# Kernel tuning notes

Hardware: AMD Instinct MI355X
Metric: run time of the kernel (lower is better)

## Reference

```python
import jax, jax.numpy as jnp
import numpy as np

N_NODES = 50000
N_EDGES = 800000
D_IN = 128
HEADS = 8
UNITS = 16


def setup_inputs() -> dict:
    key = jax.random.key(0)
    ks = jax.random.split(key, 6)
    x = jax.random.normal(ks[0], (N_NODES, D_IN), dtype=jnp.float32)
    edges = jax.random.randint(ks[1], (N_EDGES, 2), 0, N_NODES, dtype=jnp.int32)
    # glorot_uniform-style init for kernels
    lim_k = float(np.sqrt(6.0 / (D_IN + HEADS * UNITS)))
    kernel = jax.random.uniform(ks[2], (D_IN, HEADS, UNITS), minval=-lim_k, maxval=lim_k, dtype=jnp.float32)
    lim_a = float(np.sqrt(6.0 / (1 + HEADS * UNITS)))
    kernel_attention1 = jax.random.uniform(ks[3], (1, HEADS, UNITS), minval=-lim_a, maxval=lim_a, dtype=jnp.float32)
    bias_attention = jnp.zeros((1, HEADS, UNITS), dtype=jnp.float32)
    bias = jnp.zeros((HEADS * UNITS,), dtype=jnp.float32)
    return {"x": x, "edges": edges, "kernel": kernel,
            "kernel_attention1": kernel_attention1,
            "bias_attention": bias_attention, "bias": bias}


def reference(x, edges, kernel, kernel_attention1, bias_attention, bias):
    # GATv2 (version=2), merge_type='concat', use_bias=True, training=False
    n_nodes = x.shape[0]
    sources = edges[:, 0]
    targets = edges[:, 1]

    xp = jnp.einsum('nd,dhu->nhu', x, kernel)          # [N, H, U]
    xbias = xp + bias_attention                        # [N, H, U]

    # per-edge attention score: leaky_relu(x_t + x_s) . a   (GATv2)
    s = jax.nn.leaky_relu(xbias[targets] + xbias[sources], negative_slope=0.2)  # [E, H, U]
    scores = jnp.sum(s * kernel_attention1, axis=-1)   # [E, H]

    # segment softmax over incoming edges of each target node
    smax = jax.ops.segment_max(scores, targets, num_segments=n_nodes)  # [N, H]
    scores = jnp.exp(scores - smax[targets])
    ssum = jax.ops.segment_sum(scores, targets, num_segments=n_nodes)  # [N, H]
    scores = scores / (ssum[targets] + 1e-7)           # [E, H]

    # weighted scatter-aggregate of source features
    out = jax.ops.segment_sum(scores[..., None] * xp[sources], targets,
                              num_segments=n_nodes)    # [N, H, U]
    out = out.reshape(n_nodes, HEADS * UNITS) + bias   # concat heads
    return jax.nn.gelu(out, approximate=True)
```

## Files before the change

### kernel.cpp

```cpp
#include <hip/hip_runtime.h>
#include <hip/hip_fp16.h>


#define CAP 64

__device__ __forceinline__ uint2 pack_half4(float4 v) {
    __half2 a = __floats2half2_rn(v.x, v.y);
    __half2 b = __floats2half2_rn(v.z, v.w);
    uint2 r;
    r.x = *(unsigned int*)&a;
    r.y = *(unsigned int*)&b;
    return r;
}

__device__ __forceinline__ float4 unpack_half4(uint2 r) {
    __half2 a = *(__half2*)&r.x;
    __half2 b = *(__half2*)&r.y;
    const float2 fa = __half22float2(a);
    const float2 fb = __half22float2(b);
    return make_float4(fa.x, fa.y, fb.x, fb.y);
}

__device__ __forceinline__ float gelu_tanh(float x) {
    const float y = 0.7978845608028654f * fmaf(0.044715f * x, x * x, x);
    const float e = __expf(2.f * y);
    const float th = 1.f - 2.f / (e + 1.f);
    return 0.5f * x * (1.f + th);
}


__global__ __launch_bounds__(256) void gemm_scatter(
    const float* __restrict__ x, const float* __restrict__ w,
    const int* __restrict__ edges,
    unsigned short* __restrict__ xph, int* __restrict__ cnt,
    int* __restrict__ srcs, int N, int E, int gemmB) {
    __shared__ float xl[64 * 129];
    const int tid = threadIdx.x;
    const int bid = blockIdx.x;

    if (bid < gemmB) {
        const int rb = bid << 6;
        const float4* x4 = (const float4*)x;
        for (int i = tid; i < 64 * 32; i += 256) {
            const int r = i >> 5, c = i & 31;
            const int row = rb + r;
            float4 v = make_float4(0.f, 0.f, 0.f, 0.f);
            if (row < N) v = x4[(size_t)row * 32 + c];
            float* dst = &xl[r * 129 + c * 4];
            dst[0] = v.x; dst[1] = v.y; dst[2] = v.z; dst[3] = v.w;
        }
        __syncthreads();

        const int lane = tid & 63;
        const int wv = __builtin_amdgcn_readfirstlane(tid >> 6);
        const int cb = wv << 5;

        float4 acc[8];
#pragma unroll
        for (int j = 0; j < 8; ++j) acc[j] = make_float4(0.f, 0.f, 0.f, 0.f);

        const float* xrow = &xl[lane * 129];
#pragma unroll 2
        for (int k = 0; k < 128; ++k) {
            const float xv = xrow[k];
            const float4* wr = (const float4*)(w + (k << 7) + cb);
#pragma unroll
            for (int j = 0; j < 8; ++j) {
                const float4 wvv = wr[j];
                acc[j].x = fmaf(xv, wvv.x, acc[j].x);
                acc[j].y = fmaf(xv, wvv.y, acc[j].y);
                acc[j].z = fmaf(xv, wvv.z, acc[j].z);
                acc[j].w = fmaf(xv, wvv.w, acc[j].w);
            }
        }

        const int row = rb + lane;
        if (row < N) {
            uint2* o = (uint2*)(xph + (size_t)row * 128 + cb);
#pragma unroll
            for (int j = 0; j < 8; ++j) o[j] = pack_half4(acc[j]);
        }
    } else {
        const int sB = gridDim.x - gemmB;
        const int gtid = (bid - gemmB) * 256 + tid;
        const int stride = sB * 256;
        const int pairs = E >> 1;
        for (int i = gtid; i < pairs; i += stride) {
            const int4 v = ((const int4*)edges)[i];
            const int p0 = atomicAdd(&cnt[v.y], 1);
            srcs[(v.y << 6) + p0] = v.x;
            const int p1 = atomicAdd(&cnt[v.w], 1);
            srcs[(v.w << 6) + p1] = v.z;
        }
        if ((E & 1) && gtid == 0) {
            const int s = edges[(E - 1) * 2], t = edges[(E - 1) * 2 + 1];
            const int p = atomicAdd(&cnt[t], 1);
            srcs[(t << 6) + p] = s;
        }
    }
}


__device__ __forceinline__ void edge_accum4(const float4 xs, const float4 base,
                                            const float4 ka, const float mask,
                                            float4& acc, float& ssum) {
    float a0 = base.x + xs.x; a0 = fmaxf(a0, 0.2f * a0);
    float a1 = base.y + xs.y; a1 = fmaxf(a1, 0.2f * a1);
    float a2 = base.z + xs.z; a2 = fmaxf(a2, 0.2f * a2);
    float a3 = base.w + xs.w; a3 = fmaxf(a3, 0.2f * a3);
    float p = a0 * ka.x;
    p = fmaf(a1, ka.y, p);
    p = fmaf(a2, ka.z, p);
    p = fmaf(a3, ka.w, p);
    p += __shfl_xor(p, 1);
    p += __shfl_xor(p, 2);
    const float esc = __expf(p) * mask;
    acc.x = fmaf(esc, xs.x, acc.x);
    acc.y = fmaf(esc, xs.y, acc.y);
    acc.z = fmaf(esc, xs.z, acc.z);
    acc.w = fmaf(esc, xs.w, acc.w);
    ssum += esc;
}

__global__ __launch_bounds__(256) void gather_pad(
    const unsigned short* __restrict__ xph, const int* __restrict__ cnt,
    const int* __restrict__ srcs, const float* __restrict__ katt,
    const float* __restrict__ batt, const float* __restrict__ bias,
    float* __restrict__ out, int N) {
    const int node = (blockIdx.x * blockDim.x + threadIdx.x) >> 6;
    const int lane = threadIdx.x & 63;
    if (node >= N) return;
    const int c = lane & 31;
    const int half = lane >> 5;

    const int len = cnt[node];
    const int sv = srcs[(node << 6) + lane];

    const uint2* __restrict__ xp4 = (const uint2*)xph;
    const float4 xt = unpack_half4(xp4[(size_t)node * 32 + c]);
    const float4 ka = ((const float4*)katt)[c];
    const float4 ba = ((const float4*)batt)[c];
    float4 base;
    base.x = xt.x + 2.f * ba.x;
    base.y = xt.y + 2.f * ba.y;
    base.z = xt.z + 2.f * ba.z;
    base.w = xt.w + 2.f * ba.w;

    float4 acc = make_float4(0.f, 0.f, 0.f, 0.f);
    float ssum = 0.f;

    int jj = 0;
    for (; jj + 4 <= len; jj += 4) {
        const int s0 = __shfl(sv, jj + half);
        const int s1 = __shfl(sv, jj + 2 + half);
        const uint2 r0 = xp4[(size_t)s0 * 32 + c];
        const uint2 r1 = xp4[(size_t)s1 * 32 + c];
        edge_accum4(unpack_half4(r0), base, ka, 1.f, acc, ssum);
        edge_accum4(unpack_half4(r1), base, ka, 1.f, acc, ssum);
    }
    for (; jj < len; jj += 2) {
        const int j = jj + half;
        int s = __shfl(sv, j & 63);
        const bool valid = (j < len);
        s = valid ? s : 0;
        const uint2 rr = xp4[(size_t)s * 32 + c];
        edge_accum4(unpack_half4(rr), base, ka, valid ? 1.f : 0.f, acc, ssum);
    }

    acc.x += __shfl_xor(acc.x, 32);
    acc.y += __shfl_xor(acc.y, 32);
    acc.z += __shfl_xor(acc.z, 32);
    acc.w += __shfl_xor(acc.w, 32);
    ssum  += __shfl_xor(ssum, 32);

    if (half == 0) {
        const float inv = 1.f / (ssum + 1e-7f);
        const float4 b = ((const float4*)bias)[c];
        float4 o;
        o.x = gelu_tanh(fmaf(acc.x, inv, b.x));
        o.y = gelu_tanh(fmaf(acc.y, inv, b.y));
        o.z = gelu_tanh(fmaf(acc.z, inv, b.z));
        o.w = gelu_tanh(fmaf(acc.w, inv, b.w));
        ((float4*)out)[(size_t)node * 32 + c] = o;
    }
}


extern "C" void kernel_launch(void* const* d_in, const int* in_sizes, int n_in,
                              void* d_out, int out_size, void* d_ws, size_t ws_size,
                              hipStream_t stream) {
    const float* x    = (const float*)d_in[0];
    const int*   edg  = (const int*)d_in[1];
    const float* kern = (const float*)d_in[2];
    const float* katt = (const float*)d_in[3];
    const float* batt = (const float*)d_in[4];
    const float* bias = (const float*)d_in[5];

    const int N = in_sizes[0] / 128;
    const int E = in_sizes[1] / 2;

    float* out = (float*)d_out;
    unsigned short* xph = (unsigned short*)d_ws;
    int* cnt  = (int*)(xph + (size_t)N * 128);
    int* srcs = cnt + N;

    hipMemsetAsync(cnt, 0, (size_t)N * sizeof(int), stream);

    const int gemmB = (N + 63) / 64;
    const int scatB = 256;
    gemm_scatter<<<gemmB + scatB, 256, 0, stream>>>(x, kern, edg, xph, cnt, srcs,
                                                    N, E, gemmB);
    gather_pad<<<(N * 64 + 255) / 256, 256, 0, stream>>>(xph, cnt, srcs, katt,
                                                         batt, bias, out, N);
}
```

Before: 171.2 us.

## Compute projection GEMM with fp16 MFMA and fold memset into prep kernel

Replaces the scalar FP32 FMA projection with MFMA 16x16x32 f16 instructions. Each wave computes 16 rows, stages the results through shared memory and writes them out as packed fp16. A new prep kernel transposes and converts the weights to fp16 and zeroes the count array, which replaces the memset call. The scatter block count is also doubled. Inputs and weights are now rounded to fp16 before the multiply, which loses some precision, and the change adds one extra kernel launch.

After: 193.3 us. +12.9%, slower.

```diff
diff --git a/kernel.cpp b/kernel.cpp
--- a/kernel.cpp
+++ b/kernel.cpp
@@ -3,6 +3,10 @@
 
 
 #define CAP 64
+
+typedef _Float16 half_t;
+typedef __attribute__((ext_vector_type(8))) _Float16 v8h;
+typedef __attribute__((ext_vector_type(4))) float v4f;
 
 __device__ __forceinline__ uint2 pack_half4(float4 v) {
     __half2 a = __floats2half2_rn(v.x, v.y);
@@ -29,56 +33,79 @@
 }
 
 
+__global__ __launch_bounds__(256) void prep(const float* __restrict__ w,
+                                            half_t* __restrict__ wt,
+                                            int* __restrict__ cnt, int N) {
+    const int gt = blockIdx.x * 256 + threadIdx.x;
+    const int gs = gridDim.x * 256;
+    for (int i = gt; i < N; i += gs) cnt[i] = 0;
+    for (int i = gt; i < 128 * 128; i += gs) {
+        const int k = i >> 7, n = i & 127;
+        wt[(n << 7) + k] = (half_t)w[i];
+    }
+}
+
+
 __global__ __launch_bounds__(256) void gemm_scatter(
-    const float* __restrict__ x, const float* __restrict__ w,
+    const float* __restrict__ x, const half_t* __restrict__ wt,
     const int* __restrict__ edges,
     unsigned short* __restrict__ xph, int* __restrict__ cnt,
     int* __restrict__ srcs, int N, int E, int gemmB) {
-    __shared__ float xl[64 * 129];
+    __shared__ float tw[4 * 16 * 132];
     const int tid = threadIdx.x;
     const int bid = blockIdx.x;
 
     if (bid < gemmB) {
-        const int rb = bid << 6;
-        const float4* x4 = (const float4*)x;
-        for (int i = tid; i < 64 * 32; i += 256) {
-            const int r = i >> 5, c = i & 31;
-            const int row = rb + r;
-            float4 v = make_float4(0.f, 0.f, 0.f, 0.f);
-            if (row < N) v = x4[(size_t)row * 32 + c];
-            float* dst = &xl[r * 129 + c * 4];
-            dst[0] = v.x; dst[1] = v.y; dst[2] = v.z; dst[3] = v.w;
+        const int lane = tid & 63;
+        const int w4 = __builtin_amdgcn_readfirstlane(tid >> 6);
+        const int m = lane & 15;
+        const int q = lane >> 4;
+        const int rowb = (bid << 6) + (w4 << 4);
+
+        int row = rowb + m;
+        if (row >= N) row = N - 1;
+        const float* xr = x + (size_t)row * 128 + q * 8;
+
+        v8h a[4];
+#pragma unroll
+        for (int kc = 0; kc < 4; ++kc) {
+            const float4 xa = *(const float4*)(xr + kc * 32);
+            const float4 xb = *(const float4*)(xr + kc * 32 + 4);
+            v8h t;
+            t[0] = (half_t)xa.x; t[1] = (half_t)xa.y;
+            t[2] = (half_t)xa.z; t[3] = (half_t)xa.w;
+            t[4] = (half_t)xb.x; t[5] = (half_t)xb.y;
+            t[6] = (half_t)xb.z; t[7] = (half_t)xb.w;
+            a[kc] = t;
+        }
+
+        const half_t* wtb = wt + ((size_t)m << 7) + q * 8;
+        float* twr = &tw[w4 * 16 * 132];
+#pragma unroll
+        for (int nt = 0; nt < 8; ++nt) {
+            v4f acc = {0.f, 0.f, 0.f, 0.f};
+            const half_t* wn = wtb + (nt << 11);
+#pragma unroll
+            for (int kc = 0; kc < 4; ++kc) {
+                const v8h b = *(const v8h*)(wn + kc * 32);
+                acc = __builtin_amdgcn_mfma_f32_16x16x32_f16(a[kc], b, acc,
+                                                             0, 0, 0);
+            }
+#pragma unroll
+            for (int r = 0; r < 4; ++r)
+                twr[(q * 4 + r) * 132 + (nt << 4) + m] = acc[r];
         }
         __syncthreads();
 
-        const int lane = tid & 63;
-        const int wv = __builtin_amdgcn_readfirstlane(tid >> 6);
-        const int cb = wv << 5;
-
-        float4 acc[8];
-#pragma unroll
-        for (int j = 0; j < 8; ++j) acc[j] = make_float4(0.f, 0.f, 0.f, 0.f);
-
-        const float* xrow = &xl[lane * 129];
-#pragma unroll 2
-        for (int k = 0; k < 128; ++k) {
-            const float xv = xrow[k];
-            const float4* wr = (const float4*)(w + (k << 7) + cb);
-#pragma unroll
-            for (int j = 0; j < 8; ++j) {
-                const float4 wvv = wr[j];
-                acc[j].x = fmaf(xv, wvv.x, acc[j].x);
-                acc[j].y = fmaf(xv, wvv.y, acc[j].y);
-                acc[j].z = fmaf(xv, wvv.z, acc[j].z);
-                acc[j].w = fmaf(xv, wvv.w, acc[j].w);
-            }
-        }
-
-        const int row = rb + lane;
-        if (row < N) {
-            uint2* o = (uint2*)(xph + (size_t)row * 128 + cb);
-#pragma unroll
-            for (int j = 0; j < 8; ++j) o[j] = pack_half4(acc[j]);
+        const int c2 = lane & 31;
+        const int r0 = lane >> 5;
+#pragma unroll
+        for (int rp = 0; rp < 16; rp += 2) {
+            const int rr = rp + r0;
+            const float4 v = *(const float4*)&twr[rr * 132 + (c2 << 2)];
+            const int orow = rowb + rr;
+            if (orow < N)
+                *(uint2*)(xph + (size_t)orow * 128 + (c2 << 2)) = pack_half4(v);
         }
     } else {
         const int sB = gridDim.x - gemmB;
@@ -203,12 +230,13 @@
     unsigned short* xph = (unsigned short*)d_ws;
     int* cnt  = (int*)(xph + (size_t)N * 128);
     int* srcs = cnt + N;
-
-    hipMemsetAsync(cnt, 0, (size_t)N * sizeof(int), stream);
+    half_t* wt = (half_t*)(srcs + (size_t)N * CAP);
+
+    prep<<<64, 256, 0, stream>>>(kern, wt, cnt, N);
 
     const int gemmB = (N + 63) / 64;
-    const int scatB = 256;
-    gemm_scatter<<<gemmB + scatB, 256, 0, stream>>>(x, kern, edg, xph, cnt, srcs,
+    const int scatB = 512;
+    gemm_scatter<<<gemmB + scatB, 256, 0, stream>>>(x, wt, edg, xph, cnt, srcs,
                                                     N, E, gemmB);
     gather_pad<<<(N * 64 + 255) / 256, 256, 0, stream>>>(xph, cnt, srcs, katt,
                                                          batt, bias, out, N);
```
